# Optimization experiments

Hardware: AMD Instinct MI355X
Metric: run time of the kernel (lower is better)

## Reference

```python
import jax, jax.numpy as jnp
import numpy as np

S, B, D, H, DFF = 1024, 8, 1024, 16, 4096
HD = D // H
EPS = 1e-5


def layernorm(x, g, b):
    m = jnp.mean(x, axis=-1, keepdims=True)
    v = jnp.mean(jnp.square(x - m), axis=-1, keepdims=True)
    return (x - m) * jax.lax.rsqrt(v + EPS) * g + b


def setup_inputs() -> dict:
    key = jax.random.key(0)
    ks = jax.random.split(key, 6)
    w = 0.02
    return {
        "src": jax.random.normal(ks[0], (S, B, D), dtype=jnp.float32),
        "in_proj_w": jax.random.normal(ks[1], (3 * D, D), dtype=jnp.float32) * w,
        "in_proj_b": jnp.zeros((3 * D,), dtype=jnp.float32),
        "out_w": jax.random.normal(ks[2], (D, D), dtype=jnp.float32) * w,
        "out_b": jnp.zeros((D,), dtype=jnp.float32),
        "lin1_w": jax.random.normal(ks[3], (DFF, D), dtype=jnp.float32) * w,
        "lin1_b": jnp.zeros((DFF,), dtype=jnp.float32),
        "lin2_w": jax.random.normal(ks[4], (D, DFF), dtype=jnp.float32) * w,
        "lin2_b": jnp.zeros((D,), dtype=jnp.float32),
        "n1_g": jnp.ones((D,), dtype=jnp.float32),
        "n1_b": jnp.zeros((D,), dtype=jnp.float32),
        "n2_g": jnp.ones((D,), dtype=jnp.float32),
        "n2_b": jnp.zeros((D,), dtype=jnp.float32),
    }


def reference(src, in_proj_w, in_proj_b, out_w, out_b,
              lin1_w, lin1_b, lin2_w, lin2_b,
              n1_g, n1_b, n2_g, n2_b):
    # self-attention block (eval mode: dropout = identity)
    qkv = jnp.einsum('sbd,ed->sbe', src, in_proj_w) + in_proj_b  # [S,B,3D]
    q, k, v = jnp.split(qkv, 3, axis=-1)
    q = q.reshape(S, B, H, HD) * (1.0 / np.sqrt(HD)).astype(np.float32)
    k = k.reshape(S, B, H, HD)
    v = v.reshape(S, B, H, HD)
    scores = jnp.einsum('sbhd,tbhd->bhst', q, k)        # [B,H,S,S]
    attn = jax.nn.softmax(scores, axis=-1)
    o = jnp.einsum('bhst,tbhd->sbhd', attn, v).reshape(S, B, D)
    o = jnp.einsum('sbd,ed->sbe', o, out_w) + out_b
    # post-LN residuals
    x = layernorm(src + o, n1_g, n1_b)
    h = jax.nn.relu(jnp.einsum('sbd,fd->sbf', x, lin1_w) + lin1_b)
    f = jnp.einsum('sbf,df->sbd', h, lin2_w) + lin2_b
    return layernorm(x + f, n2_g, n2_b)
```

## Files before the change

kernel.cpp:

```cpp
#include <hip/hip_runtime.h>
#include <cstdint>
#include <cstddef>

#define S_  1024
#define B_  8
#define D_  1024
#define H_  16
#define HD_ 64
#define DFF_ 4096
#define M_  (S_*B_)
#define QKV_N (3*D_)

typedef float f32x4 __attribute__((ext_vector_type(4)));
typedef __bf16 bf16x8 __attribute__((ext_vector_type(8)));
typedef __bf16 bf16x4 __attribute__((ext_vector_type(4)));

#define GLDS16(gp, lp) __builtin_amdgcn_global_load_lds( \
    (__attribute__((address_space(1))) void*)(gp), \
    (__attribute__((address_space(3))) void*)(lp), 16, 0, 0)

#define CB0 (M_*D_/4)
#define CB1 (CB0 + QKV_N*D_/4)
#define CB2 (CB1 + D_*D_/4)
#define CB3 (CB2 + DFF_*D_/4)
#define CB4 (CB3 + D_*DFF_/4)

__global__ __launch_bounds__(256)
void cvt_all(const float* __restrict__ src, const float* __restrict__ w1f,
             const float* __restrict__ w2f, const float* __restrict__ w3f,
             const float* __restrict__ w4f,
             __bf16* __restrict__ src_bf, __bf16* __restrict__ w1,
             __bf16* __restrict__ w2, __bf16* __restrict__ w3,
             __bf16* __restrict__ w4)
{
    int i = blockIdx.x * 256 + threadIdx.x;
    const float* in; __bf16* out; int off;
    if      (i < CB0) { in = src; out = src_bf; off = 0;   }
    else if (i < CB1) { in = w1f; out = w1;     off = CB0; }
    else if (i < CB2) { in = w2f; out = w2;     off = CB1; }
    else if (i < CB3) { in = w3f; out = w3;     off = CB2; }
    else if (i < CB4) { in = w4f; out = w4;     off = CB3; }
    else return;
    int j = i - off;
    float4 v = *(const float4*)(in + (size_t)j * 4);
    __bf16 t[4] = {(__bf16)v.x, (__bf16)v.y, (__bf16)v.z, (__bf16)v.w};
    *(uint2*)(out + (size_t)j * 4) = *(uint2*)t;
}

template<bool OUT_BF16, bool RELU, bool ADD_BIAS, bool SPLITZ>
__global__ __launch_bounds__(512, 2)
void gemm256(const __bf16* __restrict__ A, const __bf16* __restrict__ W,
             const float* __restrict__ bias,
             void* __restrict__ Cv0, void* __restrict__ Cv1,
             int N, int Kloop, int lda)
{
    extern __shared__ __bf16 lds[];

    const int tid  = threadIdx.x;
    const int lane = tid & 63;
    const int wv   = tid >> 6;
    const int quad = lane >> 4;
    const int l15  = lane & 15;
    const int wm   = (wv >> 2) * 128;
    const int wn   = (wv & 3) * 64;

    const int id  = blockIdx.y * gridDim.x + blockIdx.x;
    const int nwg = gridDim.x * gridDim.y;
    const int q8  = nwg >> 3;
    const int k   = (id & 7) * q8 + (id >> 3);
    const int within = k & 31;
    const int chunk  = k >> 5;
    const int nchm   = gridDim.x >> 3;
    const int cm     = chunk % nchm;
    const int cn     = chunk / nchm;
    const int m0 = (cm * 8 + (within & 7)) * 256;
    const int n0 = (cn * 4 + (within >> 3)) * 256;

    void* Cv = Cv0;
    if (SPLITZ) {
        const int koff = blockIdx.z * Kloop;
        A += koff;
        W += koff;
        if (blockIdx.z) Cv = Cv1;
    }

    const int nt = Kloop >> 5;

    const int crow = tid >> 2;
    const int csl  = (tid & 3) ^ ((crow >> 1) & 3);
    const __bf16* gA0 = A + (size_t)(m0 + crow) * lda + csl * 8;
    const __bf16* gA1 = gA0 + (size_t)128 * lda;
    const __bf16* gW0 = W + (size_t)(n0 + crow) * lda + csl * 8;
    const __bf16* gW1 = gW0 + (size_t)128 * lda;
    char* ldsSt = (char*)lds + tid * 16;

    #define STAGE(kt, buf) do { \
        const int ko = (kt) << 5; \
        char* d_ = ldsSt + (buf) * 32768; \
        GLDS16(gW0 + ko, d_ + 16384); \
        GLDS16(gW1 + ko, d_ + 24576); \
        GLDS16(gA0 + ko, d_); \
        GLDS16(gA1 + ko, d_ + 8192); \
    } while (0)

    const int swz = (quad ^ ((l15 >> 1) & 3)) * 8;
    const __bf16* aBase = lds + (wm + l15) * 32 + swz;
    const __bf16* bBase = lds + 8192 + (wn + l15) * 32 + swz;

    #define RDA_ALL(arr, buf) do { const __bf16* p_ = aBase + (buf) * 16384; \
        _Pragma("unroll") for (int i_ = 0; i_ < 8; ++i_) \
            arr[i_] = *(const bf16x8*)(p_ + i_ * 512); } while (0)
    #define RDB_ALL(arr, buf) do { const __bf16* p_ = bBase + (buf) * 16384; \
        _Pragma("unroll") for (int j_ = 0; j_ < 4; ++j_) \
            arr[j_] = *(const bf16x8*)(p_ + j_ * 512); } while (0)

    #define BARRIER_DRAIN() do { \
        asm volatile("s_waitcnt vmcnt(0)" ::: "memory"); \
        __builtin_amdgcn_s_barrier(); \
        __builtin_amdgcn_sched_barrier(0); \
    } while (0)

    STAGE(0, 0);
    STAGE(1, 1);
    BARRIER_DRAIN();

    f32x4 acc[8][4] = {};
    bf16x8 aP[8], aN[8], b_[4];

    RDA_ALL(aP, 0);

    int b_cur = 0;
    for (int t = 0; t < nt; t += 2) {
        int b_nxt = b_cur + 1; if (b_nxt == 3) b_nxt = 0;
        int b_st  = b_nxt + 1; if (b_st  == 3) b_st  = 0;

        if (t + 2 < nt) STAGE(t + 2, b_st);
        RDB_ALL(b_, b_cur);
        RDA_ALL(aN, b_nxt);
        __builtin_amdgcn_s_setprio(1);
        #pragma unroll
        for (int i = 0; i < 8; ++i)
            #pragma unroll
            for (int j = 0; j < 4; ++j)
                acc[i][j] = __builtin_amdgcn_mfma_f32_16x16x32_bf16(aP[i], b_[j], acc[i][j], 0, 0, 0);
        __builtin_amdgcn_s_setprio(0);
        BARRIER_DRAIN();

        if (t + 3 < nt) STAGE(t + 3, b_cur);
        RDB_ALL(b_, b_nxt);
        if (t + 2 < nt) RDA_ALL(aP, b_st);
        __builtin_amdgcn_s_setprio(1);
        #pragma unroll
        for (int i = 0; i < 8; ++i)
            #pragma unroll
            for (int j = 0; j < 4; ++j)
                acc[i][j] = __builtin_amdgcn_mfma_f32_16x16x32_bf16(aN[i], b_[j], acc[i][j], 0, 0, 0);
        __builtin_amdgcn_s_setprio(0);
        if (t + 2 < nt) BARRIER_DRAIN();

        b_cur = b_st;
    }

    #undef BARRIER_DRAIN
    #undef RDA_ALL
    #undef RDB_ALL
    #undef STAGE

    float bvj[4];
    #pragma unroll
    for (int j = 0; j < 4; ++j)
        bvj[j] = ADD_BIAS ? bias[n0 + wn + j * 16 + l15] : 0.f;
    const size_t cbase = (size_t)(m0 + wm + quad * 4) * N + (n0 + wn + l15);
    #pragma unroll
    for (int i = 0; i < 8; ++i) {
        #pragma unroll
        for (int r = 0; r < 4; ++r) {
            const size_t rowb = cbase + (size_t)(i * 16 + r) * N;
            #pragma unroll
            for (int j = 0; j < 4; ++j) {
                float v = acc[i][j][r] + bvj[j];
                if (RELU) v = fmaxf(v, 0.f);
                if (OUT_BF16)
                    ((__bf16*)Cv)[rowb + j * 16] = (__bf16)v;
                else
                    ((float*)Cv)[rowb + j * 16] = v;
            }
        }
    }
}

__global__ __launch_bounds__(256)
void v_transpose(const __bf16* __restrict__ qkv, __bf16* __restrict__ vt)
{
    __shared__ __bf16 T[64 * 65];
    const int tid = threadIdx.x;
    const int t0  = blockIdx.x * 64;
    const int bh  = blockIdx.y;
    const int b   = bh & (B_ - 1);
    const int h   = bh / B_;

    #pragma unroll
    for (int j = 0; j < 2; ++j) {
        int c = j * 256 + tid;
        int i = c >> 3, cc = c & 7;
        const __bf16* g = qkv + (size_t)((t0 + i) * B_ + b) * QKV_N + 2 * D_ + h * HD_ + cc * 8;
        bf16x8 v = *(const bf16x8*)g;
        #pragma unroll
        for (int u = 0; u < 8; ++u) T[(cc * 8 + u) * 65 + i] = v[u];
    }
    __syncthreads();
    #pragma unroll
    for (int j = 0; j < 2; ++j) {
        int c = j * 256 + tid;
        int d = c >> 3, cc = c & 7;
        __bf16 pk[8];
        #pragma unroll
        for (int u = 0; u < 8; ++u) pk[u] = T[d * 65 + cc * 8 + u];
        *(uint4*)(vt + ((size_t)bh * HD_ + d) * S_ + t0 + cc * 8) = *(uint4*)pk;
    }
}

__global__ __launch_bounds__(512, 4)
void attn_flash(const __bf16* __restrict__ qkv, const __bf16* __restrict__ vt,
                __bf16* __restrict__ out)
{
    extern __shared__ __bf16 alds[];
    __bf16* Ks0 = alds;
    __bf16* Vs0 = alds + 16384;
    __bf16* Ps  = alds + 32768;

    const int tid  = threadIdx.x;
    const int lane = tid & 63;
    const int wv   = tid >> 6;
    const int quad = lane >> 4;
    const int l15  = lane & 15;

    const int id = blockIdx.y * gridDim.x + blockIdx.x;
    const int k  = (id & 7) * ((S_ / 128) * B_ * H_ / 8) + (id >> 3);
    const int s0 = (k & 7) * 128;
    const int bh = k >> 3;
    const int b  = bh & (B_ - 1);
    const int h  = bh / B_;

    const int i0k = tid >> 3, cck = tid & 7, scck = cck ^ (i0k & 7);
    const int i0v = tid >> 4, ccv = tid & 15, sccv = ccv ^ (i0v & 15);
    const __bf16* gK0 = qkv + ((size_t)i0k * B_ + b) * QKV_N + D_ + h * HD_ + scck * 8;
    const __bf16* gK1 = gK0 + (size_t)64 * B_ * QKV_N;
    const __bf16* gV0 = vt + ((size_t)bh * HD_ + i0v) * S_ + sccv * 8;
    const __bf16* gV1 = gV0 + (size_t)32 * S_;
    char* dK = (char*)Ks0 + tid * 16;
    char* dV = (char*)Vs0 + tid * 16;
    const size_t KADV = (size_t)128 * B_ * QKV_N;

    #define STAGEKV(buf) do { \
        GLDS16(gK0, dK + (buf) * 16384); \
        GLDS16(gK1, dK + (buf) * 16384 + 8192); \
        GLDS16(gV0, dV + (buf) * 16384); \
        GLDS16(gV1, dV + (buf) * 16384 + 8192); \
        gK0 += KADV; gK1 += KADV; gV0 += 128; gV1 += 128; \
    } while (0)

    STAGEKV(0);

    const int qrow = wv * 16 + l15;
    bf16x8 bq[2];
    #pragma unroll
    for (int kk = 0; kk < 2; ++kk)
        bq[kk] = *(const bf16x8*)(qkv + (size_t)((s0 + qrow) * B_ + b) * QKV_N
                                  + h * HD_ + kk * 32 + quad * 8);

    __syncthreads();

    f32x4 oacc[4] = {};
    float l_run = 0.f;
    const float C2 = 0.125f * 1.44269504f;
    const int xk = l15 & 7;
    const __bf16* psB = Ps + qrow * 64;

    const int nt2 = S_ / 128;
    for (int it = 0; it < nt2; ++it) {
        const int cur = it & 1;
        if (it + 1 < nt2) STAGEKV(cur ^ 1);

        #pragma unroll
        for (int s = 0; s < 2; ++s) {
            f32x4 sacc[4] = {};
            #pragma unroll
            for (int kk = 0; kk < 2; ++kk) {
                const __bf16* akB = Ks0 + cur * 8192 + s * 4096 + l15 * 64
                                    + (((kk * 4 + quad) ^ xk) * 8);
                #pragma unroll
                for (int j = 0; j < 4; ++j)
                    sacc[j] = __builtin_amdgcn_mfma_f32_16x16x32_bf16(
                        *(const bf16x8*)(akB + j * 1024), bq[kk], sacc[j], 0, 0, 0);
            }

            float rs = 0.f;
            #pragma unroll
            for (int j = 0; j < 4; ++j)
                #pragma unroll
                for (int r = 0; r < 4; ++r) {
                    float p = __builtin_amdgcn_exp2f(sacc[j][r] * C2);
                    sacc[j][r] = p;
                    rs += p;
                }
            rs += __shfl_xor(rs, 16, 64);
            rs += __shfl_xor(rs, 32, 64);
            l_run += rs;

            #pragma unroll
            for (int j = 0; j < 4; ++j) {
                __bf16 pk[4] = {(__bf16)sacc[j][0], (__bf16)sacc[j][1],
                                (__bf16)sacc[j][2], (__bf16)sacc[j][3]};
                int s16 = (j * 2 + (quad >> 1)) ^ xk;
                *(uint2*)(psB + s16 * 8 + (quad & 1) * 4) = *(uint2*)pk;
            }

            #pragma unroll
            for (int kk = 0; kk < 2; ++kk) {
                bf16x8 ap = *(const bf16x8*)(psB + (((kk * 4 + quad) ^ xk) * 8));
                const __bf16* bvB = Vs0 + cur * 8192 + l15 * 128
                                    + (((s * 8 + kk * 4 + quad) ^ l15) * 8);
                #pragma unroll
                for (int jd = 0; jd < 4; ++jd)
                    oacc[jd] = __builtin_amdgcn_mfma_f32_16x16x32_bf16(
                        ap, *(const bf16x8*)(bvB + jd * 2048), oacc[jd], 0, 0, 0);
            }
        }

        __syncthreads();
    }
    #undef STAGEKV

    float linv = 1.f / l_run;
    #pragma unroll
    for (int r = 0; r < 4; ++r) {
        float lr = __shfl(linv, quad * 4 + r, 64);
        int s = s0 + wv * 16 + quad * 4 + r;
        #pragma unroll
        for (int jd = 0; jd < 4; ++jd) {
            int d = jd * 16 + l15;
            out[(size_t)(s * B_ + b) * D_ + h * HD_ + d] = (__bf16)(oacc[jd][r] * lr);
        }
    }
}

__global__ __launch_bounds__(256)
void ln_res3(const float* __restrict__ xa, const __bf16* __restrict__ p0,
             const __bf16* __restrict__ p1, const float* __restrict__ bias,
             const float* __restrict__ g, const float* __restrict__ beta,
             float* __restrict__ yout, __bf16* __restrict__ ybf)
{
    __shared__ float red[8];
    const int row = blockIdx.x;
    const int tid = threadIdx.x;
    const size_t base = (size_t)row * D_ + tid * 4;

    float4 a  = *(const float4*)(xa + base);
    bf16x4 q0 = *(const bf16x4*)(p0 + base);
    bf16x4 q1 = *(const bf16x4*)(p1 + base);
    float4 bb = *(const float4*)(bias + tid * 4);
    float x0 = a.x + (float)q0[0] + (float)q1[0] + bb.x;
    float x1 = a.y + (float)q0[1] + (float)q1[1] + bb.y;
    float x2 = a.z + (float)q0[2] + (float)q1[2] + bb.z;
    float x3 = a.w + (float)q0[3] + (float)q1[3] + bb.w;

    float s  = x0 + x1 + x2 + x3;
    float ss = x0 * x0 + x1 * x1 + x2 * x2 + x3 * x3;
    for (int msk = 1; msk <= 32; msk <<= 1) {
        s  += __shfl_xor(s,  msk, 64);
        ss += __shfl_xor(ss, msk, 64);
    }
    const int wv = tid >> 6;
    if ((tid & 63) == 0) { red[wv] = s; red[4 + wv] = ss; }
    __syncthreads();
    s  = red[0] + red[1] + red[2] + red[3];
    ss = red[4] + red[5] + red[6] + red[7];
    float mean = s * (1.f / D_);
    float var  = ss * (1.f / D_) - mean * mean;
    float rstd = rsqrtf(var + 1e-5f);

    float4 gv = *(const float4*)(g + tid * 4);
    float4 bv = *(const float4*)(beta + tid * 4);
    float y0 = (x0 - mean) * rstd * gv.x + bv.x;
    float y1 = (x1 - mean) * rstd * gv.y + bv.y;
    float y2 = (x2 - mean) * rstd * gv.z + bv.z;
    float y3 = (x3 - mean) * rstd * gv.w + bv.w;
    *(float4*)(yout + base) = make_float4(y0, y1, y2, y3);
    if (ybf) {
        __bf16 t[4] = {(__bf16)y0, (__bf16)y1, (__bf16)y2, (__bf16)y3};
        *(uint2*)(ybf + base) = *(uint2*)t;
    }
}

extern "C" void kernel_launch(void* const* d_in, const int* in_sizes, int n_in,
                              void* d_out, int out_size, void* d_ws, size_t ws_size,
                              hipStream_t stream)
{
    const float* src       = (const float*)d_in[0];
    const float* in_proj_w = (const float*)d_in[1];
    const float* in_proj_b = (const float*)d_in[2];
    const float* out_w     = (const float*)d_in[3];
    const float* out_b     = (const float*)d_in[4];
    const float* lin1_w    = (const float*)d_in[5];
    const float* lin1_b    = (const float*)d_in[6];
    const float* lin2_w    = (const float*)d_in[7];
    const float* lin2_b    = (const float*)d_in[8];
    const float* n1_g = (const float*)d_in[9];
    const float* n1_b = (const float*)d_in[10];
    const float* n2_g = (const float*)d_in[11];
    const float* n2_b = (const float*)d_in[12];

    char* ws = (char*)d_ws;
    size_t off = 0;
    auto alloc = [&](size_t bytes) { char* p = ws + off; off += (bytes + 255) & ~(size_t)255; return p; };

    __bf16* src_bf = (__bf16*)alloc((size_t)M_ * D_ * 2);
    __bf16* w1     = (__bf16*)alloc((size_t)QKV_N * D_ * 2);
    __bf16* w2     = (__bf16*)alloc((size_t)D_ * D_ * 2);
    __bf16* w3     = (__bf16*)alloc((size_t)DFF_ * D_ * 2);
    __bf16* w4     = (__bf16*)alloc((size_t)D_ * DFF_ * 2);
    __bf16* qkv    = (__bf16*)alloc((size_t)M_ * QKV_N * 2);
    char*   h_r    = alloc((size_t)M_ * DFF_ * 2);
    __bf16* xbf    = (__bf16*)alloc((size_t)M_ * D_ * 2);
    float*  xf     = (float*)alloc((size_t)M_ * D_ * 4);
    __bf16* vt     = (__bf16*)alloc((size_t)B_ * H_ * HD_ * S_ * 2);

    const size_t PART = (size_t)M_ * D_;
    __bf16* attn_o = src_bf;
    __bf16* o0 = (__bf16*)h_r;
    __bf16* o1 = o0 + PART;
    __bf16* hbf = (__bf16*)h_r;
    __bf16* f0 = vt;
    __bf16* f1 = xbf;

    const size_t SHM  = 98304;
    const size_t ASHM = 81920;

    cvt_all<<<(CB4 + 255) / 256, 256, 0, stream>>>(
        src, in_proj_w, out_w, lin1_w, lin2_w, src_bf, w1, w2, w3, w4);

    gemm256<true, false, true, false><<<dim3(M_ / 256, QKV_N / 256), 512, SHM, stream>>>(
        src_bf, w1, in_proj_b, qkv, nullptr, QKV_N, D_, D_);

    v_transpose<<<dim3(S_ / 64, B_ * H_), 256, 0, stream>>>(qkv, vt);

    attn_flash<<<dim3(S_ / 128, B_ * H_), 512, ASHM, stream>>>(qkv, vt, attn_o);

    gemm256<true, false, false, true><<<dim3(M_ / 256, D_ / 256, 2), 512, SHM, stream>>>(
        attn_o, w2, nullptr, o0, o1, D_, D_ / 2, D_);

    ln_res3<<<M_, 256, 0, stream>>>(src, o0, o1, out_b, n1_g, n1_b, xf, xbf);

    gemm256<true, true, true, false><<<dim3(M_ / 256, DFF_ / 256), 512, SHM, stream>>>(
        xbf, w3, lin1_b, hbf, nullptr, DFF_, D_, D_);

    gemm256<true, false, false, true><<<dim3(M_ / 256, D_ / 256, 2), 512, SHM, stream>>>(
        hbf, w4, nullptr, f0, f1, D_, DFF_ / 2, DFF_);

    ln_res3<<<M_, 256, 0, stream>>>(xf, f0, f1, lin2_b, n2_g, n2_b, (float*)d_out, nullptr);
}
```

Before: 457.5 us.

## Add 128x256-tile GEMM kernel and use it for QKV projection

Introduces a gemm128 kernel with 128x256 output tiles, a K-step of 32, double-buffered LDS (48KB) and launch bounds allowing 4 blocks per CU, and switches the QKV projection to it. The grid doubles along M to 64x12 blocks, which covers the CUs better than the 32x12 grid of the 256x256 kernel. The trade-off is less operand reuse per tile, more global traffic, and a simpler pipeline with a full barrier on every K step.

```diff
diff --git a/kernel.cpp b/kernel.cpp
--- a/kernel.cpp
+++ b/kernel.cpp
@@ -173,6 +173,124 @@
     const size_t cbase = (size_t)(m0 + wm + quad * 4) * N + (n0 + wn + l15);
     #pragma unroll
     for (int i = 0; i < 8; ++i) {
+        #pragma unroll
+        for (int r = 0; r < 4; ++r) {
+            const size_t rowb = cbase + (size_t)(i * 16 + r) * N;
+            #pragma unroll
+            for (int j = 0; j < 4; ++j) {
+                float v = acc[i][j][r] + bvj[j];
+                if (RELU) v = fmaxf(v, 0.f);
+                if (OUT_BF16)
+                    ((__bf16*)Cv)[rowb + j * 16] = (__bf16)v;
+                else
+                    ((float*)Cv)[rowb + j * 16] = v;
+            }
+        }
+    }
+}
+
+template<bool OUT_BF16, bool RELU, bool ADD_BIAS, bool SPLITZ>
+__global__ __launch_bounds__(512, 4)
+void gemm128(const __bf16* __restrict__ A, const __bf16* __restrict__ W,
+             const float* __restrict__ bias,
+             void* __restrict__ Cv0, void* __restrict__ Cv1,
+             int N, int Kloop, int lda)
+{
+    extern __shared__ __bf16 lds[];
+
+    const int tid  = threadIdx.x;
+    const int lane = tid & 63;
+    const int wv   = tid >> 6;
+    const int quad = lane >> 4;
+    const int l15  = lane & 15;
+    const int wm   = (wv & 1) * 64;
+    const int wn   = (wv >> 1) * 64;
+
+    const int id  = blockIdx.y * gridDim.x + blockIdx.x;
+    const int nwg = gridDim.x * gridDim.y;
+    const int q8  = nwg >> 3;
+    const int k   = (id & 7) * q8 + (id >> 3);
+    const int within = k & 31;
+    const int chunk  = k >> 5;
+    const int nchm   = gridDim.x >> 3;
+    const int cm     = chunk % nchm;
+    const int cn     = chunk / nchm;
+    const int m0 = (cm * 8 + (within & 7)) * 128;
+    const int n0 = (cn * 4 + (within >> 3)) * 256;
+
+    void* Cv = Cv0;
+    if (SPLITZ) {
+        const int koff = blockIdx.z * Kloop;
+        A += koff;
+        W += koff;
+        if (blockIdx.z) Cv = Cv1;
+    }
+
+    const int nt = Kloop >> 5;
+
+    const int crow = tid >> 2;
+    const int csl  = (tid & 3) ^ ((crow >> 1) & 3);
+    const __bf16* gA0 = A + (size_t)(m0 + crow) * lda + csl * 8;
+    const __bf16* gW0 = W + (size_t)(n0 + crow) * lda + csl * 8;
+    const __bf16* gW1 = gW0 + (size_t)128 * lda;
+    char* ldsSt = (char*)lds + tid * 16;
+
+    #define STAGE(kt, buf) do { \
+        const int ko = (kt) << 5; \
+        char* d_ = ldsSt + (buf) * 24576; \
+        GLDS16(gW0 + ko, d_ + 8192); \
+        GLDS16(gW1 + ko, d_ + 16384); \
+        GLDS16(gA0 + ko, d_); \
+    } while (0)
+
+    const int swz = (quad ^ ((l15 >> 1) & 3)) * 8;
+    const __bf16* aBase = lds + (wm + l15) * 32 + swz;
+    const __bf16* bBase = lds + 4096 + (wn + l15) * 32 + swz;
+
+    #define BARRIER_DRAIN() do { \
+        asm volatile("s_waitcnt vmcnt(0)" ::: "memory"); \
+        __builtin_amdgcn_s_barrier(); \
+        __builtin_amdgcn_sched_barrier(0); \
+    } while (0)
+
+    STAGE(0, 0);
+    BARRIER_DRAIN();
+
+    f32x4 acc[4][4] = {};
+
+    for (int t = 0; t < nt; ++t) {
+        const int cur = t & 1;
+        if (t + 1 < nt) STAGE(t + 1, cur ^ 1);
+
+        const __bf16* aB = aBase + cur * 12288;
+        const __bf16* bB = bBase + cur * 12288;
+        bf16x8 b_[4];
+        #pragma unroll
+        for (int j = 0; j < 4; ++j)
+            b_[j] = *(const bf16x8*)(bB + j * 512);
+        __builtin_amdgcn_s_setprio(1);
+        #pragma unroll
+        for (int i = 0; i < 4; ++i) {
+            bf16x8 a_ = *(const bf16x8*)(aB + i * 512);
+            #pragma unroll
+            for (int j = 0; j < 4; ++j)
+                acc[i][j] = __builtin_amdgcn_mfma_f32_16x16x32_bf16(a_, b_[j], acc[i][j], 0, 0, 0);
+        }
+        __builtin_amdgcn_s_setprio(0);
+
+        if (t + 1 < nt) BARRIER_DRAIN();
+    }
+
+    #undef BARRIER_DRAIN
+    #undef STAGE
+
+    float bvj[4];
+    #pragma unroll
+    for (int j = 0; j < 4; ++j)
+        bvj[j] = ADD_BIAS ? bias[n0 + wn + j * 16 + l15] : 0.f;
+    const size_t cbase = (size_t)(m0 + wm + quad * 4) * N + (n0 + wn + l15);
+    #pragma unroll
+    for (int i = 0; i < 4; ++i) {
         #pragma unroll
         for (int r = 0; r < 4; ++r) {
             const size_t rowb = cbase + (size_t)(i * 16 + r) * N;
@@ -434,13 +552,14 @@
     __bf16* f0 = vt;
     __bf16* f1 = xbf;
 
-    const size_t SHM  = 98304;
-    const size_t ASHM = 81920;
+    const size_t SHM   = 98304;
+    const size_t SHM2  = 49152;
+    const size_t ASHM  = 81920;
 
     cvt_all<<<(CB4 + 255) / 256, 256, 0, stream>>>(
         src, in_proj_w, out_w, lin1_w, lin2_w, src_bf, w1, w2, w3, w4);
 
-    gemm256<true, false, true, false><<<dim3(M_ / 256, QKV_N / 256), 512, SHM, stream>>>(
+    gemm128<true, false, true, false><<<dim3(M_ / 128, QKV_N / 256), 512, SHM2, stream>>>(
         src_bf, w1, in_proj_b, qkv, nullptr, QKV_N, D_, D_);
 
     v_transpose<<<dim3(S_ / 64, B_ * H_), 256, 0, stream>>>(qkv, vt);
```

New measurement: 443.7 us. 3.0% less time.
